# Kernel tuning notes

Measured on AMD Instinct MI355X. Metric: run time of the kernel, lower is better.

Reference implementation:

```python
import jax, jax.numpy as jnp
import numpy as np

RF = 16       # receptive_field
STRIDE = 16   # sim_strides
ALPHA = 0.3   # tf.keras LeakyReLU default alpha
EPS = 1e-3    # tf.keras BatchNormalization default epsilon


def _leaky(x):
    return jnp.where(x > 0, x, ALPHA * x)


def _bn_train(x, gamma, beta):
    # training-mode batch norm over (B, H, W), channel-last
    mu = jnp.mean(x, axis=(0, 1, 2))
    var = jnp.var(x, axis=(0, 1, 2))
    return (x - mu) * jax.lax.rsqrt(var + EPS) * gamma + beta


def _cbl(x, W, gamma, beta):
    # 1x1 conv (== channel matmul) + BN + LeakyReLU
    y = jnp.einsum('bhwc,cd->bhwd', x, W)
    return _leaky(_bn_train(y, gamma, beta))


def setup_inputs() -> dict:
    key = jax.random.key(0)
    ks = jax.random.split(key, 4)
    B, H, Wd, C = 4, 64, 64, 256
    s = 1.0 / np.sqrt(C)
    return {
        'inputs': jax.random.normal(ks[0], (B, H, Wd, C), jnp.float32),
        'Wq': jax.random.normal(ks[1], (C, C), jnp.float32) * s,
        'gq': jnp.ones((C,), jnp.float32), 'bq': jnp.zeros((C,), jnp.float32),
        'Wk': jax.random.normal(ks[2], (C, C), jnp.float32) * s,
        'gk': jnp.ones((C,), jnp.float32), 'bk': jnp.zeros((C,), jnp.float32),
        'Wv': jax.random.normal(ks[3], (C, C), jnp.float32) * s,
        'gv': jnp.ones((C,), jnp.float32), 'bv': jnp.zeros((C,), jnp.float32),
        'g1': jnp.ones((C,), jnp.float32), 'b1': jnp.zeros((C,), jnp.float32),
    }


def _windows(x):
    # x: [B,H,W,C] -> [B, nH*nW, RF, RF, C] overlapping-capable window gather
    H, Wd = x.shape[1], x.shape[2]
    nH = (H - RF) // STRIDE + 1
    nW = (Wd - RF) // STRIDE + 1
    ih = (jnp.arange(nH) * STRIDE)[:, None] + jnp.arange(RF)[None, :]  # [nH,RF]
    iw = (jnp.arange(nW) * STRIDE)[:, None] + jnp.arange(RF)[None, :]  # [nW,RF]
    xw = x[:, ih][:, :, :, iw]            # [B,nH,RF,nW,RF,C]
    xw = xw.transpose(0, 1, 3, 2, 4, 5)   # [B,nH,nW,RF,RF,C]
    return xw.reshape(x.shape[0], nH * nW, RF, RF, x.shape[3])


def reference(inputs, Wq, gq, bq, Wk, gk, bk, Wv, gv, bv, g1, b1):
    Q = _cbl(inputs, Wq, gq, bq)   # [B,H,W,C]
    K = _cbl(inputs, Wk, gk, bk)
    V = _cbl(inputs, Wv, gv, bv)
    C = Q.shape[-1]
    Kw = _windows(K)               # [B,N,RF,RF,C]
    Vw = _windows(V)
    # full-Q x window-K attention, summed over windows (matches nested loop)
    scores = jnp.einsum('bijc,bnpqc->bnijpq', Q, Kw) / jnp.sqrt(jnp.asarray(C, Q.dtype))
    scores = _leaky(scores)
    yout = jnp.einsum('bnijpq,bnpqc->bijc', scores, Vw)  # sum over windows n
    y = _bn_train(yout, g1, b1)
    # softmax jointly over spatial axes (1,2)
    m = jnp.max(y, axis=(1, 2), keepdims=True)
    e = jnp.exp(y - m)
    return e / jnp.sum(e, axis=(1, 2), keepdims=True)
```

## Files before the change

### kernel.cpp

```cpp
#include <hip/hip_runtime.h>
#include <stdint.h>


typedef __attribute__((ext_vector_type(8)))  short short8;
typedef __attribute__((ext_vector_type(4)))  float f32x4;
typedef __attribute__((ext_vector_type(16))) float f32x16;
typedef __attribute__((ext_vector_type(4)))  unsigned short ushort4v;

#define ALPHA 0.3f
#define EPS   1e-3
#define NTOT  16384.0

__device__ __forceinline__ unsigned short f2bf(float f){
  unsigned u = __float_as_uint(f);
  u += 0x7FFFu + ((u>>16)&1u);
  return (unsigned short)(u>>16);
}
__device__ __forceinline__ float lrelu(float x){ return x > 0.f ? x : ALPHA*x; }

__global__ __launch_bounds__(256)
void k_cvt(const float* __restrict__ X, unsigned short* __restrict__ Xb){
  int i = (blockIdx.x*256 + threadIdx.x)*4;
  float4 v = *(const float4*)(X + i);
  ushort4v o; o.x = f2bf(v.x); o.y = f2bf(v.y); o.z = f2bf(v.z); o.w = f2bf(v.w);
  *(ushort4v*)(Xb + i) = o;
}

__global__ __launch_bounds__(256)
void k_wtrans(const float* __restrict__ Wq,
              const float* __restrict__ Wk,
              const float* __restrict__ Wv,
              unsigned short* __restrict__ Wt){
  int o = blockIdx.x*256 + threadIdx.x;
  int p = o >> 16, rem = o & 65535;
  int j = rem >> 8, c = rem & 255;
  const float* W = (p==0) ? Wq : ((p==1) ? Wk : Wv);
  Wt[o] = f2bf(W[c*256 + j]);
}

__global__ __launch_bounds__(256)
void k_qkv_gemm(const unsigned short* __restrict__ X,
                const unsigned short* __restrict__ Wt,
                float* __restrict__ Y){
  __shared__ __align__(16) unsigned short At[64*264];
  __shared__ __align__(16) unsigned short Bt[64*264];
  int tid = threadIdx.x;
  int mb = blockIdx.x, nb = blockIdx.y;
#pragma unroll
  for (int it = 0; it < 8; ++it){
    int s = it*256 + tid;
    int row = s >> 5, ch = s & 31;
    uint4 a = *(const uint4*)(X  + ((size_t)(mb*64 + row))*256 + ch*8);
    uint4 b = *(const uint4*)(Wt + ((size_t)(nb*64 + row))*256 + ch*8);
    *(uint4*)(At + row*264 + ch*8) = a;
    *(uint4*)(Bt + row*264 + ch*8) = b;
  }
  __syncthreads();
  int lane = tid & 63, wv = tid >> 6;
  int ln15 = lane & 15, quad = lane >> 4;
  int rw = (wv & 1)*32, cw = (wv >> 1)*32;
  f32x4 acc[2][2] = {};
#pragma unroll
  for (int ks = 0; ks < 8; ++ks){
    short8 afr[2], bfr[2];
#pragma unroll
    for (int mt = 0; mt < 2; ++mt){
      int r = rw + mt*16 + ln15;
      afr[mt] = *(const short8*)(At + r*264 + (ks*4+quad)*8);
    }
#pragma unroll
    for (int nt = 0; nt < 2; ++nt){
      int r = cw + nt*16 + ln15;
      bfr[nt] = *(const short8*)(Bt + r*264 + (ks*4+quad)*8);
    }
#pragma unroll
    for (int mt = 0; mt < 2; ++mt)
#pragma unroll
      for (int nt = 0; nt < 2; ++nt)
        acc[mt][nt] = __builtin_amdgcn_mfma_f32_16x16x32_bf16(afr[mt], bfr[nt], acc[mt][nt], 0,0,0);
  }
#pragma unroll
  for (int mt = 0; mt < 2; ++mt)
#pragma unroll
    for (int nt = 0; nt < 2; ++nt)
#pragma unroll
      for (int r = 0; r < 4; ++r){
        int row = mb*64 + rw + mt*16 + quad*4 + r;
        int col = nb*64 + cw + nt*16 + ln15;
        Y[(size_t)row*768 + col] = acc[mt][nt][r];
      }
}

__global__ __launch_bounds__(256)
void k_stats1(const float* __restrict__ Y, double* __restrict__ st){
  int tid = threadIdx.x;
  int r0 = blockIdx.x * 32;
  float sum[3] = {0,0,0}, sq[3] = {0,0,0};
#pragma unroll 4
  for (int r = 0; r < 32; ++r){
    const float* row = Y + (size_t)(r0 + r)*768;
#pragma unroll
    for (int cg = 0; cg < 3; ++cg){
      float v = row[cg*256 + tid];
      sum[cg] += v; sq[cg] += v*v;
    }
  }
#pragma unroll
  for (int cg = 0; cg < 3; ++cg){
    atomicAdd(&st[cg*256 + tid], (double)sum[cg]);
    atomicAdd(&st[768 + cg*256 + tid], (double)sq[cg]);
  }
}

__global__ __launch_bounds__(256)
void k_coef(const double* __restrict__ st,
            const float* __restrict__ gq, const float* __restrict__ bq,
            const float* __restrict__ gk, const float* __restrict__ bk,
            const float* __restrict__ gv, const float* __restrict__ bv,
            float* __restrict__ scv, float* __restrict__ shv){
  int cc = blockIdx.x*256 + threadIdx.x;
  int proj = cc >> 8, c = cc & 255;
  double mu  = st[cc]     * (1.0/NTOT);
  double var = st[768+cc] * (1.0/NTOT) - mu*mu;
  double g = (proj==0) ? gq[c] : (proj==1) ? gk[c] : gv[c];
  double b = (proj==0) ? bq[c] : (proj==1) ? bk[c] : bv[c];
  double sc = g / sqrt(var + EPS);
  scv[cc] = (float)sc;
  shv[cc] = (float)(b - mu*sc);
}

__global__ __launch_bounds__(256)
void k_bn_qk(const float* __restrict__ Y,
             const float* __restrict__ scv, const float* __restrict__ shv,
             unsigned short* __restrict__ Qf, unsigned short* __restrict__ Kf){
  int idx = blockIdx.x*256 + threadIdx.x;
  int t = idx >> 6, cb = idx & 63;
  int proj = cb >> 5, cbl = cb & 31;
  int ch0 = cbl*8;
  const float* src = Y + (size_t)t*768 + proj*256 + ch0;
  float4 v0 = *(const float4*)(src);
  float4 v1 = *(const float4*)(src + 4);
  const float* sc = scv + proj*256 + ch0;
  const float* sh = shv + proj*256 + ch0;
  unsigned short r[8];
  r[0]=f2bf(lrelu(v0.x*sc[0]+sh[0])); r[1]=f2bf(lrelu(v0.y*sc[1]+sh[1]));
  r[2]=f2bf(lrelu(v0.z*sc[2]+sh[2])); r[3]=f2bf(lrelu(v0.w*sc[3]+sh[3]));
  r[4]=f2bf(lrelu(v1.x*sc[4]+sh[4])); r[5]=f2bf(lrelu(v1.y*sc[5]+sh[5]));
  r[6]=f2bf(lrelu(v1.z*sc[6]+sh[6])); r[7]=f2bf(lrelu(v1.w*sc[7]+sh[7]));
  uint4 u;
  u.x = (unsigned)r[0] | ((unsigned)r[1]<<16);
  u.y = (unsigned)r[2] | ((unsigned)r[3]<<16);
  u.z = (unsigned)r[4] | ((unsigned)r[5]<<16);
  u.w = (unsigned)r[6] | ((unsigned)r[7]<<16);
  int g = t >> 5, l31r = t & 31;
  int ks = cbl >> 1, l5c = cbl & 1;
  unsigned short* dst = (proj ? Kf : Qf) + ((size_t)((g*16 + ks)*64 + l5c*32 + l31r))*8;
  *(uint4*)dst = u;
}

__global__ __launch_bounds__(256)
void k_bn_v(const float* __restrict__ Y,
            const float* __restrict__ scv, const float* __restrict__ shv,
            unsigned short* __restrict__ Vf){
  __shared__ unsigned short tile[64][66];
  int tid = threadIdx.x;
  int pt = blockIdx.x, ct = blockIdx.y, b = blockIdx.z;
  int cl = tid & 63, rq = tid >> 6;
  int c  = ct*64 + cl;
  float sc = scv[512 + c], sh = shv[512 + c];
#pragma unroll 4
  for (int k = 0; k < 16; ++k){
    int r = k*4 + rq;
    size_t t = (size_t)b*4096 + pt*64 + r;
    float v = Y[t*768 + 512 + c];
    tile[r][cl] = f2bf(lrelu(v*sc + sh));
  }
  __syncthreads();
#pragma unroll
  for (int it = 0; it < 2; ++it){
    int m = it*256 + tid;
    int c2 = m >> 3, kg = m & 7;
    int ch = ct*64 + c2;
    int gc = b*8 + (ch >> 5), l31c = ch & 31;
    int kp = pt*4 + (kg >> 1), l5k = kg & 1;
    unsigned short r0 = tile[kg*8+0][c2], r1 = tile[kg*8+1][c2];
    unsigned short r2 = tile[kg*8+2][c2], r3 = tile[kg*8+3][c2];
    unsigned short r4 = tile[kg*8+4][c2], r5 = tile[kg*8+5][c2];
    unsigned short r6 = tile[kg*8+6][c2], r7 = tile[kg*8+7][c2];
    uint4 u;
    u.x = (unsigned)r0 | ((unsigned)r1<<16);
    u.y = (unsigned)r2 | ((unsigned)r3<<16);
    u.z = (unsigned)r4 | ((unsigned)r5<<16);
    u.w = (unsigned)r6 | ((unsigned)r7<<16);
    *(uint4*)(Vf + ((size_t)((gc*256 + kp)*64 + l5k*32 + l31c))*8) = u;
  }
}

__global__ __launch_bounds__(512, 4)
void k_attn(const unsigned short* __restrict__ Qf,
            const unsigned short* __restrict__ Kf,
            const unsigned short* __restrict__ Vf,
            float* __restrict__ P0, float* __restrict__ P1){
  __shared__ __align__(16) unsigned short Ql[64*256];
  __shared__ __align__(16) unsigned short Sl[64*264];
  int tid = threadIdx.x;
  int blk = blockIdx.x;
  int qt = blk >> 3, combo = blk & 7;
  int b = combo >> 1, half = combo & 1;
  int q0 = qt*64;
  int lane = tid & 63, w = tid >> 6;
  int l31 = lane & 31, l5 = lane >> 5;
  float* P = half ? P1 : P0;

  int gq0 = b*128 + qt*2;
  {
    const uint4* src = (const uint4*)(Qf + (size_t)gq0*8192);
    uint4* dst = (uint4*)Ql;
#pragma unroll
    for (int it = 0; it < 4; ++it) dst[it*512 + tid] = src[it*512 + tid];
  }
  __syncthreads();

  f32x16 acc2[2] = {};
  int gk0 = b*128 + half*64 + w;
  const unsigned short* kb = Kf + (size_t)gk0*8192 + lane*8;
  const unsigned short* vb = Vf + ((size_t)((b*8 + w)*256 + half*128))*512 + lane*8;
  const unsigned short* qa0 = Ql + lane*8;
  const unsigned short* qa1 = Ql + 16*512 + lane*8;

  for (int kt = 0; kt < 8; ++kt){
    f32x16 a1[2] = {};
    const unsigned short* kbt = kb + (size_t)kt*8*8192;
#pragma unroll
    for (int ks = 0; ks < 16; ++ks){
      short8 kf = *(const short8*)(kbt + ks*512);
      short8 q0v = *(const short8*)(qa0 + ks*512);
      short8 q1v = *(const short8*)(qa1 + ks*512);
      a1[0] = __builtin_amdgcn_mfma_f32_32x32x16_bf16(q0v, kf, a1[0], 0, 0, 0);
      a1[1] = __builtin_amdgcn_mfma_f32_32x32x16_bf16(q1v, kf, a1[1], 0, 0, 0);
    }
    __syncthreads();
#pragma unroll
    for (int reg = 0; reg < 16; ++reg){
      int rloc = (reg & 3) + 8*(reg >> 2) + 4*l5;
      Sl[rloc*264 + w*32 + l31]        = f2bf(lrelu(a1[0][reg]*0.0625f));
      Sl[(32 + rloc)*264 + w*32 + l31] = f2bf(lrelu(a1[1][reg]*0.0625f));
    }
    __syncthreads();
    const unsigned short* vbt = vb + (size_t)kt*16*512;
#pragma unroll
    for (int kk = 0; kk < 16; ++kk){
      short8 vf = *(const short8*)(vbt + kk*512);
      short8 s0 = *(const short8*)(Sl + (     l31)*264 + kk*16 + l5*8);
      short8 s1 = *(const short8*)(Sl + (32 + l31)*264 + kk*16 + l5*8);
      acc2[0] = __builtin_amdgcn_mfma_f32_32x32x16_bf16(s0, vf, acc2[0], 0, 0, 0);
      acc2[1] = __builtin_amdgcn_mfma_f32_32x32x16_bf16(s1, vf, acc2[1], 0, 0, 0);
    }
  }
#pragma unroll
  for (int c = 0; c < 2; ++c)
#pragma unroll
    for (int reg = 0; reg < 16; ++reg){
      int row = q0 + c*32 + (reg & 3) + 8*(reg >> 2) + 4*l5;
      P[((size_t)b*4096 + row)*256 + w*32 + l31] = acc2[c][reg];
    }
}

__global__ __launch_bounds__(256)
void k_red(const float* __restrict__ P0, const float* __restrict__ P1,
           float* __restrict__ yout, double* __restrict__ st){
  int tid = threadIdx.x;
  int r0 = blockIdx.x*32;
  double sum = 0, sq = 0;
#pragma unroll 4
  for (int r = 0; r < 32; ++r){
    size_t idx = (size_t)(r0 + r)*256 + tid;
    float v = P0[idx] + P1[idx];
    yout[idx] = v;
    sum += v; sq += (double)v*v;
  }
  atomicAdd(&st[1536 + tid], sum);
  atomicAdd(&st[1792 + tid], sq);
}

__global__ __launch_bounds__(256)
void k_soft1(const float* __restrict__ yout, const double* __restrict__ st,
             const float* __restrict__ g1, float* __restrict__ sums){
  __shared__ float red[256];
  __shared__ float sA[64], sK[64];
  int tid = threadIdx.x;
  int chunk = blockIdx.x, ct = blockIdx.y, b = blockIdx.z;
  int cl = tid & 63, pg = tid >> 6;
  int c = ct*64 + cl;
  if (tid < 64){
    int cc = ct*64 + tid;
    double mu  = st[1536 + cc]*(1.0/NTOT);
    double var = st[1792 + cc]*(1.0/NTOT) - mu*mu;
    double a = g1[cc] / sqrt(var + EPS);
    sA[tid] = (float)a;
    sK[tid] = (float)(a*mu);
  }
  __syncthreads();
  float a = sA[cl], K = sK[cl];
  float s = 0.f;
  const float* base = yout + ((size_t)b*4096 + chunk*256)*256 + c;
#pragma unroll 4
  for (int k = 0; k < 64; ++k){
    float v = base[(size_t)(pg + k*4)*256];
    s += __expf(v*a - K);
  }
  red[tid] = s;
  __syncthreads();
  if (tid < 64){
    float tot = red[tid] + red[64+tid] + red[128+tid] + red[192+tid];
    atomicAdd(&sums[b*256 + ct*64 + tid], tot);
  }
}

__global__ __launch_bounds__(256)
void k_soft2(const float* __restrict__ yout, const double* __restrict__ st,
             const float* __restrict__ g1, const float* __restrict__ sums,
             float* __restrict__ out){
  __shared__ float sA[64], sK[64], sR[64];
  int tid = threadIdx.x;
  int chunk = blockIdx.x, ct = blockIdx.y, b = blockIdx.z;
  int cl = tid & 63, pg = tid >> 6;
  int c = ct*64 + cl;
  if (tid < 64){
    int cc = ct*64 + tid;
    double mu  = st[1536 + cc]*(1.0/NTOT);
    double var = st[1792 + cc]*(1.0/NTOT) - mu*mu;
    double a = g1[cc] / sqrt(var + EPS);
    sA[tid] = (float)a;
    sK[tid] = (float)(a*mu);
    sR[tid] = 1.f / sums[b*256 + cc];
  }
  __syncthreads();
  float a = sA[cl], K = sK[cl], rl = sR[cl];
  const float* base = yout + ((size_t)b*4096 + chunk*256)*256 + c;
  float* obase = out + ((size_t)b*4096 + chunk*256)*256 + c;
#pragma unroll 4
  for (int k = 0; k < 64; ++k){
    size_t idx = (size_t)(pg + k*4)*256;
    obase[idx] = __expf(base[idx]*a - K) * rl;
  }
}

extern "C" void kernel_launch(void* const* d_in, const int* in_sizes, int n_in,
                              void* d_out, int out_size, void* d_ws, size_t ws_size,
                              hipStream_t stream){
  (void)in_sizes; (void)n_in; (void)out_size; (void)ws_size;
  const float* X  = (const float*)d_in[0];
  const float* Wq = (const float*)d_in[1];
  const float* gq = (const float*)d_in[2];
  const float* bq = (const float*)d_in[3];
  const float* Wk = (const float*)d_in[4];
  const float* gk = (const float*)d_in[5];
  const float* bk = (const float*)d_in[6];
  const float* Wv = (const float*)d_in[7];
  const float* gv = (const float*)d_in[8];
  const float* bv = (const float*)d_in[9];
  const float* g1 = (const float*)d_in[10];

  char* ws = (char*)d_ws;
  double*         st   = (double*)ws;
  float*          sums = (float*)(ws + 16384);
  float*          scv  = (float*)(ws + 20480);
  float*          shv  = (float*)(ws + 23552);
  unsigned short* Wt   = (unsigned short*)(ws + 26624);
  unsigned short* Xb   = (unsigned short*)(ws + 419840);
  float*          Y    = (float*)(ws + 8808448);
  unsigned short* Kf   = (unsigned short*)(ws + 59140096);
  unsigned short* Vf   = (unsigned short*)(ws + 67528704);
  unsigned short* Qf   = Xb;
  float*          P0   = Y;
  float*          P1   = (float*)((char*)Y + 16777216);
  float*          yo   = (float*)((char*)Y + 33554432);

  hipMemsetAsync(st, 0, 20480, stream);
  k_cvt     <<<4096, 256, 0, stream>>>(X, Xb);
  k_wtrans  <<<768, 256, 0, stream>>>(Wq, Wk, Wv, Wt);
  k_qkv_gemm<<<dim3(256,12), 256, 0, stream>>>(Xb, Wt, Y);
  k_stats1  <<<512, 256, 0, stream>>>(Y, st);
  k_coef    <<<3, 256, 0, stream>>>(st, gq, bq, gk, bk, gv, bv, scv, shv);
  k_bn_qk   <<<4096, 256, 0, stream>>>(Y, scv, shv, Qf, Kf);
  k_bn_v    <<<dim3(64,4,4), 256, 0, stream>>>(Y, scv, shv, Vf);
  k_attn    <<<512, 512, 0, stream>>>(Qf, Kf, Vf, P0, P1);
  k_red     <<<512, 256, 0, stream>>>(P0, P1, yo, st);
  k_soft1   <<<dim3(16,4,4), 256, 0, stream>>>(yo, st, g1, sums);
  k_soft2   <<<dim3(16,4,4), 256, 0, stream>>>(yo, st, g1, sums, (float*)d_out);
}
```

Measured before the change: 252.8 us.

## Fuse BN stats into QKV GEMM, write Q/K in fragment layout, add setprio

The QKV GEMM epilogue now reduces per-column sum and sum-of-squares through shared-memory atomics and then global double atomics, which removes the separate stats kernel and its full reread of Y. Q/K outputs are written straight into the MFMA fragment order, so the BN kernel becomes a contiguous streaming pass, and V goes to its own compact buffer. The attention MFMA loops gain s_setprio hints, and the final reduce kernel uses fewer, larger blocks. The risks are strided scattered stores in the GEMM epilogue and extra atomic traffic.

```diff
diff --git a/kernel.cpp b/kernel.cpp
--- a/kernel.cpp
+++ b/kernel.cpp
@@ -41,7 +41,8 @@
 __global__ __launch_bounds__(256)
 void k_qkv_gemm(const unsigned short* __restrict__ X,
                 const unsigned short* __restrict__ Wt,
-                float* __restrict__ Y){
+                float* __restrict__ YQK, float* __restrict__ Yv,
+                double* __restrict__ st){
   __shared__ __align__(16) unsigned short At[64*264];
   __shared__ __align__(16) unsigned short Bt[64*264];
   int tid = threadIdx.x;
@@ -79,36 +80,61 @@
       for (int nt = 0; nt < 2; ++nt)
         acc[mt][nt] = __builtin_amdgcn_mfma_f32_16x16x32_bf16(afr[mt], bfr[nt], acc[mt][nt], 0,0,0);
   }
+  float ps[2] = {0.f, 0.f}, pq[2] = {0.f, 0.f};
 #pragma unroll
   for (int mt = 0; mt < 2; ++mt)
 #pragma unroll
     for (int nt = 0; nt < 2; ++nt)
 #pragma unroll
       for (int r = 0; r < 4; ++r){
-        int row = mb*64 + rw + mt*16 + quad*4 + r;
-        int col = nb*64 + cw + nt*16 + ln15;
-        Y[(size_t)row*768 + col] = acc[mt][nt][r];
+        float v = acc[mt][nt][r];
+        ps[nt] += v; pq[nt] += v*v;
       }
-}
-
-__global__ __launch_bounds__(256)
-void k_stats1(const float* __restrict__ Y, double* __restrict__ st){
-  int tid = threadIdx.x;
-  int r0 = blockIdx.x * 32;
-  float sum[3] = {0,0,0}, sq[3] = {0,0,0};
-#pragma unroll 4
-  for (int r = 0; r < 32; ++r){
-    const float* row = Y + (size_t)(r0 + r)*768;
-#pragma unroll
-    for (int cg = 0; cg < 3; ++cg){
-      float v = row[cg*256 + tid];
-      sum[cg] += v; sq[cg] += v*v;
-    }
-  }
-#pragma unroll
-  for (int cg = 0; cg < 3; ++cg){
-    atomicAdd(&st[cg*256 + tid], (double)sum[cg]);
-    atomicAdd(&st[768 + cg*256 + tid], (double)sq[cg]);
+  if (nb < 8){
+    int proj = nb >> 2;
+    float* base = YQK + (size_t)proj*(16384*256);
+    int l5c = ln15 >> 3, j = ln15 & 7;
+#pragma unroll
+    for (int mt = 0; mt < 2; ++mt){
+      int g = (mb*64 + rw + mt*16) >> 5;
+      int l31r0 = ((rw + mt*16) & 31) + quad*4;
+#pragma unroll
+      for (int nt = 0; nt < 2; ++nt){
+        int ks2 = ((nb & 3)*64 + cw + nt*16) >> 4;
+#pragma unroll
+        for (int r = 0; r < 4; ++r){
+          size_t chunk = (size_t)((g*16 + ks2)*64 + l5c*32 + l31r0 + r);
+          base[chunk*8 + j] = acc[mt][nt][r];
+        }
+      }
+    }
+  } else {
+    int vc0 = (nb - 8)*64 + cw;
+#pragma unroll
+    for (int mt = 0; mt < 2; ++mt)
+#pragma unroll
+      for (int nt = 0; nt < 2; ++nt)
+#pragma unroll
+        for (int r = 0; r < 4; ++r){
+          int row = mb*64 + rw + mt*16 + quad*4 + r;
+          Yv[(size_t)row*256 + vc0 + nt*16 + ln15] = acc[mt][nt][r];
+        }
+  }
+  __syncthreads();
+  float* red = (float*)At;
+  if (tid < 128) red[tid] = 0.f;
+  __syncthreads();
+#pragma unroll
+  for (int nt = 0; nt < 2; ++nt){
+    int colL = cw + nt*16 + ln15;
+    atomicAdd(&red[colL],      ps[nt]);
+    atomicAdd(&red[64 + colL], pq[nt]);
+  }
+  __syncthreads();
+  if (tid < 64){
+    int cc = nb*64 + tid;
+    atomicAdd(&st[cc],       (double)red[tid]);
+    atomicAdd(&st[768 + cc], (double)red[64 + tid]);
   }
 }
 
@@ -130,14 +156,15 @@
 }
 
 __global__ __launch_bounds__(256)
-void k_bn_qk(const float* __restrict__ Y,
+void k_bn_qk(const float* __restrict__ YQK,
              const float* __restrict__ scv, const float* __restrict__ shv,
              unsigned short* __restrict__ Qf, unsigned short* __restrict__ Kf){
-  int idx = blockIdx.x*256 + threadIdx.x;
-  int t = idx >> 6, cb = idx & 63;
-  int proj = cb >> 5, cbl = cb & 31;
-  int ch0 = cbl*8;
-  const float* src = Y + (size_t)t*768 + proj*256 + ch0;
+  int oc = blockIdx.x*256 + threadIdx.x;
+  int proj = oc >> 19;
+  int rest = oc & 524287;
+  int ks = (rest >> 6) & 15, l5c = (rest >> 5) & 1;
+  int ch0 = ks*16 + l5c*8;
+  const float* src = YQK + (size_t)oc*8;
   float4 v0 = *(const float4*)(src);
   float4 v1 = *(const float4*)(src + 4);
   const float* sc = scv + proj*256 + ch0;
@@ -152,14 +179,11 @@
   u.y = (unsigned)r[2] | ((unsigned)r[3]<<16);
   u.z = (unsigned)r[4] | ((unsigned)r[5]<<16);
   u.w = (unsigned)r[6] | ((unsigned)r[7]<<16);
-  int g = t >> 5, l31r = t & 31;
-  int ks = cbl >> 1, l5c = cbl & 1;
-  unsigned short* dst = (proj ? Kf : Qf) + ((size_t)((g*16 + ks)*64 + l5c*32 + l31r))*8;
-  *(uint4*)dst = u;
-}
-
-__global__ __launch_bounds__(256)
-void k_bn_v(const float* __restrict__ Y,
+  *(uint4*)((proj ? Kf : Qf) + (size_t)rest*8) = u;
+}
+
+__global__ __launch_bounds__(256)
+void k_bn_v(const float* __restrict__ Yv,
             const float* __restrict__ scv, const float* __restrict__ shv,
             unsigned short* __restrict__ Vf){
   __shared__ unsigned short tile[64][66];
@@ -172,7 +196,7 @@
   for (int k = 0; k < 16; ++k){
     int r = k*4 + rq;
     size_t t = (size_t)b*4096 + pt*64 + r;
-    float v = Y[t*768 + 512 + c];
+    float v = Yv[t*256 + c];
     tile[r][cl] = f2bf(lrelu(v*sc + sh));
   }
   __syncthreads();
@@ -231,6 +255,7 @@
   for (int kt = 0; kt < 8; ++kt){
     f32x16 a1[2] = {};
     const unsigned short* kbt = kb + (size_t)kt*8*8192;
+    __builtin_amdgcn_s_setprio(1);
 #pragma unroll
     for (int ks = 0; ks < 16; ++ks){
       short8 kf = *(const short8*)(kbt + ks*512);
@@ -239,6 +264,7 @@
       a1[0] = __builtin_amdgcn_mfma_f32_32x32x16_bf16(q0v, kf, a1[0], 0, 0, 0);
       a1[1] = __builtin_amdgcn_mfma_f32_32x32x16_bf16(q1v, kf, a1[1], 0, 0, 0);
     }
+    __builtin_amdgcn_s_setprio(0);
     __syncthreads();
 #pragma unroll
     for (int reg = 0; reg < 16; ++reg){
@@ -248,6 +274,7 @@
     }
     __syncthreads();
     const unsigned short* vbt = vb + (size_t)kt*16*512;
+    __builtin_amdgcn_s_setprio(1);
 #pragma unroll
     for (int kk = 0; kk < 16; ++kk){
       short8 vf = *(const short8*)(vbt + kk*512);
@@ -256,6 +283,7 @@
       acc2[0] = __builtin_amdgcn_mfma_f32_32x32x16_bf16(s0, vf, acc2[0], 0, 0, 0);
       acc2[1] = __builtin_amdgcn_mfma_f32_32x32x16_bf16(s1, vf, acc2[1], 0, 0, 0);
     }
+    __builtin_amdgcn_s_setprio(0);
   }
 #pragma unroll
   for (int c = 0; c < 2; ++c)
@@ -270,10 +298,10 @@
 void k_red(const float* __restrict__ P0, const float* __restrict__ P1,
            float* __restrict__ yout, double* __restrict__ st){
   int tid = threadIdx.x;
-  int r0 = blockIdx.x*32;
+  int r0 = blockIdx.x*128;
   double sum = 0, sq = 0;
 #pragma unroll 4
-  for (int r = 0; r < 32; ++r){
+  for (int r = 0; r < 128; ++r){
     size_t idx = (size_t)(r0 + r)*256 + tid;
     float v = P0[idx] + P1[idx];
     yout[idx] = v;
@@ -369,24 +397,24 @@
   float*          shv  = (float*)(ws + 23552);
   unsigned short* Wt   = (unsigned short*)(ws + 26624);
   unsigned short* Xb   = (unsigned short*)(ws + 419840);
-  float*          Y    = (float*)(ws + 8808448);
+  float*          YQK  = (float*)(ws + 8808448);
+  float*          Yv   = (float*)(ws + 42362880);
   unsigned short* Kf   = (unsigned short*)(ws + 59140096);
   unsigned short* Vf   = (unsigned short*)(ws + 67528704);
   unsigned short* Qf   = Xb;
-  float*          P0   = Y;
-  float*          P1   = (float*)((char*)Y + 16777216);
-  float*          yo   = (float*)((char*)Y + 33554432);
+  float*          P0   = YQK;
+  float*          P1   = (float*)((char*)YQK + 16777216);
+  float*          yo   = Yv;
 
   hipMemsetAsync(st, 0, 20480, stream);
   k_cvt     <<<4096, 256, 0, stream>>>(X, Xb);
   k_wtrans  <<<768, 256, 0, stream>>>(Wq, Wk, Wv, Wt);
-  k_qkv_gemm<<<dim3(256,12), 256, 0, stream>>>(Xb, Wt, Y);
-  k_stats1  <<<512, 256, 0, stream>>>(Y, st);
+  k_qkv_gemm<<<dim3(256,12), 256, 0, stream>>>(Xb, Wt, YQK, Yv, st);
   k_coef    <<<3, 256, 0, stream>>>(st, gq, bq, gk, bk, gv, bv, scv, shv);
-  k_bn_qk   <<<4096, 256, 0, stream>>>(Y, scv, shv, Qf, Kf);
-  k_bn_v    <<<dim3(64,4,4), 256, 0, stream>>>(Y, scv, shv, Vf);
+  k_bn_qk   <<<4096, 256, 0, stream>>>(YQK, scv, shv, Qf, Kf);
+  k_bn_v    <<<dim3(64,4,4), 256, 0, stream>>>(Yv, scv, shv, Vf);
   k_attn    <<<512, 512, 0, stream>>>(Qf, Kf, Vf, P0, P1);
-  k_red     <<<512, 256, 0, stream>>>(P0, P1, yo, st);
+  k_red     <<<128, 256, 0, stream>>>(P0, P1, yo, st);
   k_soft1   <<<dim3(16,4,4), 256, 0, stream>>>(yo, st, g1, sums);
   k_soft2   <<<dim3(16,4,4), 256, 0, stream>>>(yo, st, g1, sums, (float*)d_out);
 }
```

Measured after the change: 252.4 us. Within noise of the previous version (-0.2%).
